# Optimization experiments

Hardware: AMD Instinct MI355X
Metric: run time of the kernel (lower is better)

The kernel has to match this reference:

```python
import jax, jax.numpy as jnp
import numpy as np

B, DIM, MID, H, W = 4, 256, 128, 128, 128
EPS = 1e-5


def _conv(x, w, pad):
    # x: [B,C,H,W], w: [O,I,k,k]
    return jax.lax.conv_general_dilated(
        x, w, window_strides=(1, 1), padding=[(pad, pad), (pad, pad)],
        dimension_numbers=('NCHW', 'OIHW', 'NCHW'))


def _bn(x, g, b, m, v):
    inv = jax.lax.rsqrt(v + EPS)
    scale = (g * inv)[None, :, None, None]
    shift = (b - m * g * inv)[None, :, None, None]
    return x * scale + shift


def _convbnrelu(x, w, g, b, m, v):
    return jax.nn.relu(_bn(_conv(x, w, 1), g, b, m, v))


# CornerNet directional pools: sequential max-accumulation scans.
def top_pool(x):     # max over y' >= y  -> reversed cummax along H
    return jax.lax.cummax(x, axis=2, reverse=True)

def bottom_pool(x):  # max over y' <= y
    return jax.lax.cummax(x, axis=2)

def left_pool(x):    # max over x' >= x
    return jax.lax.cummax(x, axis=3, reverse=True)

def right_pool(x):   # max over x' <= x
    return jax.lax.cummax(x, axis=3)


def setup_inputs() -> dict:
    key = jax.random.key(0)
    ks = jax.random.split(key, 32)
    it = iter(ks)

    def w(shape, scale=0.05):
        return jax.random.normal(next(it), shape, jnp.float32) * scale

    def bn_params(c):
        return (jnp.ones((c,), jnp.float32) + 0.1 * jax.random.normal(next(it), (c,), jnp.float32),
                0.1 * jax.random.normal(next(it), (c,), jnp.float32),
                0.1 * jax.random.normal(next(it), (c,), jnp.float32),
                jax.random.uniform(next(it), (c,), jnp.float32) + 0.5)

    inp = {'x': jax.random.normal(next(it), (B, DIM, H, W), jnp.float32)}

    inp['p1_w'] = w((MID, DIM, 3, 3))
    inp['p1_g'], inp['p1_b'], inp['p1_m'], inp['p1_v'] = bn_params(MID)
    inp['p2_w'] = w((MID, DIM, 3, 3))
    inp['p2_g'], inp['p2_b'], inp['p2_m'], inp['p2_v'] = bn_params(MID)
    inp['p_w'] = w((DIM, MID, 3, 3))
    inp['p_g'], inp['p_b'], inp['p_m'], inp['p_v'] = bn_params(DIM)
    inp['c1_w'] = w((DIM, DIM, 1, 1))
    inp['c1_g'], inp['c1_b'], inp['c1_m'], inp['c1_v'] = bn_params(DIM)
    inp['c2_w'] = w((DIM, DIM, 3, 3))
    inp['c2_g'], inp['c2_b'], inp['c2_m'], inp['c2_v'] = bn_params(DIM)
    return inp


def reference(x,
              p1_w, p1_g, p1_b, p1_m, p1_v,
              p2_w, p2_g, p2_b, p2_m, p2_v,
              p_w, p_g, p_b, p_m, p_v,
              c1_w, c1_g, c1_b, c1_m, c1_v,
              c2_w, c2_g, c2_b, c2_m, c2_v):
    # branch 1: conv-bn-relu -> top pool -> bottom pool
    pool1 = bottom_pool(top_pool(_convbnrelu(x, p1_w, p1_g, p1_b, p1_m, p1_v)))
    # branch 2: conv-bn-relu -> left pool -> right pool
    pool2 = right_pool(left_pool(_convbnrelu(x, p2_w, p2_g, p2_b, p2_m, p2_v)))
    # merge branch
    p_bn1 = _bn(_conv(pool1 + pool2, p_w, 1), p_g, p_b, p_m, p_v)
    # skip branch: 1x1 conv + bn
    bn1 = _bn(_conv(x, c1_w, 0), c1_g, c1_b, c1_m, c1_v)
    # residual add + relu, then final conv-bn-relu
    return _convbnrelu(jax.nn.relu(p_bn1 + bn1), c2_w, c2_g, c2_b, c2_m, c2_v)
```

## Files before the change

kernel.cpp:

```cpp
#include <hip/hip_runtime.h>
#include <hip/hip_bf16.h>
#include <math.h>


constexpr int NB   = 4;
constexpr int CDIM = 256;
constexpr int CMID = 128;
constexpr int HS   = 128;
constexpr int WS   = 128;
constexpr float EPS = 1e-5f;

typedef __bf16 bf16x8 __attribute__((ext_vector_type(8)));
typedef float  f32x4  __attribute__((ext_vector_type(4)));

#define AS1 __attribute__((address_space(1)))
#define AS3 __attribute__((address_space(3)))

__device__ __forceinline__ void load16_lds(const void* gsrc, void* ldst) {
    __builtin_amdgcn_global_load_lds((const AS1 unsigned int*)gsrc,
                                     (AS3 unsigned int*)ldst, 16, 0, 0);
}

__global__ __launch_bounds__(512) void k_xprep(const float* __restrict__ xin,
                                               __hip_bfloat16* __restrict__ Xc)
{
    const int y = blockIdx.x;
    const int b = blockIdx.y;
    const int t = threadIdx.x;
    __shared__ __hip_bfloat16 lds[128 * 264];
#pragma unroll
    for (int k = 0; k < 16; ++k) {
        int idx = t + k * 512;
        int ci = idx >> 5, x4 = idx & 31;
        f32x4 v = *(const f32x4*)(xin + (((size_t)b * CDIM + ci) * HS + y) * WS + x4 * 4);
#pragma unroll
        for (int j = 0; j < 4; ++j)
            lds[(x4 * 4 + j) * 264 + ci] = __float2bfloat16(v[j]);
    }
    __syncthreads();
#pragma unroll
    for (int k = 0; k < 8; ++k) {
        int i = t + k * 512;
        int x = i >> 5, c8 = i & 31;
        bf16x8 vv = *(const bf16x8*)(lds + x * 264 + c8 * 8);
        *(bf16x8*)(Xc + ((size_t)(b * 128 + y) * 128 + x) * 256 + c8 * 8) = vv;
    }
}

__global__ __launch_bounds__(256) void k_wprep_all(
    const float* __restrict__ p1w, const float* __restrict__ p2w,
    const float* __restrict__ c2w, const float* __restrict__ c1w,
    __hip_bfloat16* __restrict__ Aw1, __hip_bfloat16* __restrict__ Aw2,
    __hip_bfloat16* __restrict__ Aw5, __hip_bfloat16* __restrict__ Aw4)
{
    const int bid = blockIdx.x;
    const int t   = threadIdx.x;
    if (bid < 512) {
        const float* W; __hip_bfloat16* A; int co;
        if (bid < 128)      { W = p1w; A = Aw1; co = bid; }
        else if (bid < 256) { W = p2w; A = Aw2; co = bid - 128; }
        else                { W = c2w; A = Aw5; co = bid - 256; }
#pragma unroll
        for (int tap = 0; tap < 9; ++tap)
            A[(size_t)co * 2304 + tap * 256 + t] =
                __float2bfloat16(W[((size_t)co * CDIM + t) * 9 + tap]);
    } else {
        int base = (bid - 512) * 512 + t;
        Aw4[base]       = __float2bfloat16(c1w[base]);
        Aw4[base + 256] = __float2bfloat16(c1w[base + 256]);
    }
}

template<int MODE>
__global__ __launch_bounds__(256, 2) void k_conv3(
    const __hip_bfloat16* __restrict__ Xc,
    const __hip_bfloat16* __restrict__ Aw,
    const float* __restrict__ zbuf,
    const float* __restrict__ gg, const float* __restrict__ bbp,
    const float* __restrict__ mmp, const float* __restrict__ vvp,
    void* __restrict__ outp, int CO)
{
    const int y   = blockIdx.x;
    const int co0 = blockIdx.y * 128;
    const int b   = blockIdx.z;

    __shared__ __hip_bfloat16 smem[514 * 64];
    __shared__ float s_sc[128], s_sh[128];
    __shared__ unsigned s_red[128];
    char* smb = (char*)smem;

    const int t    = threadIdx.x;
    const int lane = t & 63;
    const int w    = t >> 6;
    const int ml   = lane & 15;
    const int q    = lane >> 4;
    const int mbase = (w >> 1) * 64;
    const int nbase = (w & 1) * 64;

    if (t < 128) {
        int co = co0 + t;
        float iv = rsqrtf(vvp[co] + EPS);
        float sc = gg[co] * iv;
        s_sc[t] = sc;
        s_sh[t] = bbp[co] - mmp[co] * sc;
        if (MODE == 2) s_red[t] = 0u;
    }

    f32x4 acc[4][4];
#pragma unroll
    for (int mt = 0; mt < 4; ++mt)
#pragma unroll
        for (int nt = 0; nt < 4; ++nt)
            acc[mt][nt] = (f32x4){0.f, 0.f, 0.f, 0.f};

#pragma unroll 1
    for (int ky = 0; ky < 3; ++ky) {
        const int ydata = y + ky - 1;
        if ((unsigned)ydata >= 128u) continue;
        const __hip_bfloat16* arow = Aw + (size_t)co0 * 2304 + (3 * ky) * 256;
        const __hip_bfloat16* brow = Xc + (size_t)(b * 128 + ydata) * 128 * 256;
#pragma unroll 1
        for (int cih = 0; cih < 4; ++cih) {
#pragma unroll
            for (int p = 0; p < 17; ++p) {
                int i = t + p * 256;
                if (i < 4112) {
                    int row = i >> 3;
                    int cl  = (i & 7) ^ (row & 7);
                    const __hip_bfloat16* src;
                    if (row < 384) {
                        int j    = row >> 7;
                        int co_l = row & 127;
                        src = arow + (size_t)co_l * 2304 + j * 256 + cih * 64 + cl * 8;
                    } else {
                        int gx = (row - 384) - 1;
                        src = ((unsigned)gx < 128u)
                            ? brow + (size_t)gx * 256 + cih * 64 + cl * 8
                            : (const __hip_bfloat16*)((const char*)zbuf + cl * 16);
                    }
                    load16_lds(src, smb + (size_t)i * 16);
                }
            }
            __syncthreads();
#pragma unroll
            for (int j = 0; j < 3; ++j) {
#pragma unroll
                for (int s = 0; s < 2; ++s) {
                    bf16x8 af[4], bfv[4];
#pragma unroll
                    for (int mt = 0; mt < 4; ++mt) {
                        const int ra = j * 128 + mbase + mt * 16 + ml;
                        const int coff = ((s * 4 + q) ^ (ra & 7)) * 16;
                        af[mt] = *(const bf16x8*)(smb + (size_t)ra * 128 + coff);
                    }
#pragma unroll
                    for (int nt = 0; nt < 4; ++nt) {
                        const int rb = 384 + nbase + nt * 16 + ml + j;
                        const int coff = ((s * 4 + q) ^ (rb & 7)) * 16;
                        bfv[nt] = *(const bf16x8*)(smb + (size_t)rb * 128 + coff);
                    }
#pragma unroll
                    for (int mt = 0; mt < 4; ++mt)
#pragma unroll
                        for (int nt = 0; nt < 4; ++nt)
                            acc[mt][nt] = __builtin_amdgcn_mfma_f32_16x16x32_bf16(
                                af[mt], bfv[nt], acc[mt][nt], 0, 0, 0);
                }
            }
            __syncthreads();
        }
    }

#pragma unroll
    for (int mt = 0; mt < 4; ++mt) {
#pragma unroll
        for (int r = 0; r < 4; ++r) {
            const int col = mbase + mt * 16 + q * 4 + r;
            const float sc = s_sc[col], sh = s_sh[col];
            const int co = co0 + col;
            unsigned rmx = 0u;
#pragma unroll
            for (int nt = 0; nt < 4; ++nt) {
                float v = fmaxf(acc[mt][nt][r] * sc + sh, 0.f);
                const int x = nbase + nt * 16 + ml;
                if (MODE == 0) {
                    ((float*)outp)[(((size_t)b * CO + co) * HS + y) * WS + x] = v;
                } else if (MODE == 1) {
                    atomicMax((unsigned*)outp + ((size_t)(b * 128 + co)) * 128 + x,
                              __float_as_uint(v));
                } else {
                    rmx = max(rmx, __float_as_uint(v));
                }
            }
            if (MODE == 2) atomicMax(&s_red[col], rmx);
        }
    }
    if (MODE == 2) {
        __syncthreads();
        if (t < 128)
            atomicMax((unsigned*)outp + ((size_t)(b * 128 + t)) * 128 + y, s_red[t]);
    }
}

__global__ __launch_bounds__(128) void k_uv(
    const float* __restrict__ pw, const float* __restrict__ cm,
    const float* __restrict__ rm,
    __hip_bfloat16* __restrict__ U, __hip_bfloat16* __restrict__ V)
{
    const int co   = blockIdx.x;
    const int b    = blockIdx.y;
    const int mode = blockIdx.z;
    const int p    = threadIdx.x;
    float acc0 = 0.f, acc1 = 0.f, acc2 = 0.f;
    const float* base = (mode == 0) ? cm : rm;
    for (int ci = 0; ci < CMID; ++ci) {
        const float* w9 = pw + (co * CMID + ci) * 9;
        float s0[3], s1[3], s2[3];
        if (mode == 0) {
#pragma unroll
            for (int k = 0; k < 3; ++k) {
                float a = w9[k], qq = w9[3 + k], r = w9[6 + k];
                s0[k] = qq + r; s1[k] = a + qq + r; s2[k] = a + qq;
            }
        } else {
#pragma unroll
            for (int k = 0; k < 3; ++k) {
                float a = w9[k*3 + 0], qq = w9[k*3 + 1], r = w9[k*3 + 2];
                s0[k] = qq + r; s1[k] = a + qq + r; s2[k] = a + qq;
            }
        }
        const float* v = base + (b * CMID + ci) * 128;
#pragma unroll
        for (int k = 0; k < 3; ++k) {
            int pos = p + k - 1;
            if ((unsigned)pos < 128u) {
                float vv = v[pos];
                acc0 += s0[k] * vv; acc1 += s1[k] * vv; acc2 += s2[k] * vv;
            }
        }
    }
    __hip_bfloat16* dst = (mode == 0) ? U : V;
    dst[((0 * NB + b) * CDIM + co) * 128 + p] = __float2bfloat16(acc0);
    dst[((1 * NB + b) * CDIM + co) * 128 + p] = __float2bfloat16(acc1);
    dst[((2 * NB + b) * CDIM + co) * 128 + p] = __float2bfloat16(acc2);
}

__global__ __launch_bounds__(256, 3) void k_merge_mfma(
    const __hip_bfloat16* __restrict__ Xc, const __hip_bfloat16* __restrict__ Aw4,
    const __hip_bfloat16* __restrict__ U, const __hip_bfloat16* __restrict__ V,
    const float* __restrict__ pg, const float* __restrict__ pb,
    const float* __restrict__ pm, const float* __restrict__ pv,
    const float* __restrict__ cg, const float* __restrict__ cb,
    const float* __restrict__ cmn, const float* __restrict__ cv,
    __hip_bfloat16* __restrict__ Rc)
{
    const int y   = blockIdx.x;
    const int cot = blockIdx.y;
    const int b   = blockIdx.z;
    const int co0 = cot * 128;
    __shared__ __hip_bfloat16 smem[256 * 64];
    __shared__ float s_psc[128], s_psh[128], s_csc[128], s_csh[128];
    __shared__ float s_v0[128], s_vm[128], s_v1[128];
    char* smb = (char*)smem;
    const int t = threadIdx.x, lane = t & 63, w = t >> 6;
    const int ml = lane & 15, q = lane >> 4;
    const int mbase = (w >> 1) * 64, nbase = (w & 1) * 64;
    const int yc = (y == 0) ? 0 : ((y == HS - 1) ? 2 : 1);

    if (t < 128) {
        int co = co0 + t;
        float iv = rsqrtf(pv[co] + EPS);
        float psc = pg[co] * iv;
        s_psc[t] = psc;
        s_psh[t] = pb[co] - pm[co] * psc;
        float iv2 = rsqrtf(cv[co] + EPS);
        float csc = cg[co] * iv2;
        s_csc[t] = csc;
        s_csh[t] = cb[co] - cmn[co] * csc;
        const size_t vb = ((size_t)b * CDIM + co) * 128 + y;
        const size_t cstr = (size_t)NB * CDIM * 128;
        s_v0[t] = __bfloat162float(V[vb]);
        s_vm[t] = __bfloat162float(V[cstr + vb]);
        s_v1[t] = __bfloat162float(V[2 * cstr + vb]);
    }

    f32x4 acc[4][4];
#pragma unroll
    for (int mt = 0; mt < 4; ++mt)
#pragma unroll
        for (int nt = 0; nt < 4; ++nt)
            acc[mt][nt] = (f32x4){0.f, 0.f, 0.f, 0.f};

    const __hip_bfloat16* brow = Xc + (size_t)(b * 128 + y) * 128 * 256;
#pragma unroll 1
    for (int ks = 0; ks < 4; ++ks) {
        const __hip_bfloat16* ab = Aw4 + (size_t)co0 * 256 + ks * 64;
        const __hip_bfloat16* bb = brow + ks * 64;
#pragma unroll
        for (int p = 0; p < 8; ++p) {
            int i   = t + p * 256;
            int row = i >> 3;
            int c   = (i & 7) ^ (row & 7);
            const __hip_bfloat16* src = (row < 128)
                ? ab + (size_t)row * 256 + c * 8
                : bb + (size_t)(row - 128) * 256 + c * 8;
            load16_lds(src, smb + (size_t)i * 16);
        }
        __syncthreads();
#pragma unroll
        for (int s = 0; s < 2; ++s) {
            const int coff = ((s * 4 + q) ^ (ml & 7)) * 16;
            bf16x8 af[4], bfv[4];
#pragma unroll
            for (int mt = 0; mt < 4; ++mt)
                af[mt] = *(const bf16x8*)(smb + (size_t)(mbase + mt * 16 + ml) * 128 + coff);
#pragma unroll
            for (int nt = 0; nt < 4; ++nt)
                bfv[nt] = *(const bf16x8*)(smb + (size_t)(128 + nbase + nt * 16 + ml) * 128 + coff);
#pragma unroll
            for (int mt = 0; mt < 4; ++mt)
#pragma unroll
                for (int nt = 0; nt < 4; ++nt)
                    acc[mt][nt] = __builtin_amdgcn_mfma_f32_16x16x32_bf16(
                        af[mt], bfv[nt], acc[mt][nt], 0, 0, 0);
        }
        __syncthreads();
    }

    const __hip_bfloat16* Ub = U + ((size_t)(yc * NB + b) * CDIM + co0) * 128;
#pragma unroll
    for (int p = 0; p < 8; ++p) {
        int i = t + p * 256;
        load16_lds(Ub + (size_t)i * 8, smb + (size_t)i * 16);
    }
    __syncthreads();

#pragma unroll
    for (int mt = 0; mt < 4; ++mt) {
#pragma unroll
        for (int nt = 0; nt < 4; ++nt) {
            const int x = nbase + nt * 16 + ml;
            unsigned long long pk = 0;
#pragma unroll
            for (int r = 0; r < 4; ++r) {
                const int col = mbase + mt * 16 + q * 4 + r;
                float u  = __bfloat162float(smem[col * 128 + x]);
                float vt = (x == 0) ? s_v0[col] : ((x == WS - 1) ? s_v1[col] : s_vm[col]);
                float val = fmaxf((u + vt) * s_psc[col] + s_psh[col]
                                  + acc[mt][nt][r] * s_csc[col] + s_csh[col], 0.f);
                __hip_bfloat16 hb = __float2bfloat16(val);
                unsigned short bits;
                __builtin_memcpy(&bits, &hb, 2);
                pk |= (unsigned long long)bits << (16 * r);
            }
            *(unsigned long long*)((char*)Rc +
                ((size_t)((b * 128 + y) * 128 + x) * 256 + co0 + mbase + mt * 16 + q * 4) * 2) = pk;
        }
    }
}

extern "C" void kernel_launch(void* const* d_in, const int* in_sizes, int n_in,
                              void* d_out, int out_size, void* d_ws, size_t ws_size,
                              hipStream_t stream)
{
    (void)in_sizes; (void)n_in; (void)out_size; (void)ws_size;
    const float* x    = (const float*)d_in[0];
    const float* p1_w = (const float*)d_in[1];
    const float* p1_g = (const float*)d_in[2];
    const float* p1_b = (const float*)d_in[3];
    const float* p1_m = (const float*)d_in[4];
    const float* p1_v = (const float*)d_in[5];
    const float* p2_w = (const float*)d_in[6];
    const float* p2_g = (const float*)d_in[7];
    const float* p2_b = (const float*)d_in[8];
    const float* p2_m = (const float*)d_in[9];
    const float* p2_v = (const float*)d_in[10];
    const float* p_w  = (const float*)d_in[11];
    const float* p_g  = (const float*)d_in[12];
    const float* p_b  = (const float*)d_in[13];
    const float* p_m  = (const float*)d_in[14];
    const float* p_v  = (const float*)d_in[15];
    const float* c1_w = (const float*)d_in[16];
    const float* c1_g = (const float*)d_in[17];
    const float* c1_b = (const float*)d_in[18];
    const float* c1_m = (const float*)d_in[19];
    const float* c1_v = (const float*)d_in[20];
    const float* c2_w = (const float*)d_in[21];
    const float* c2_g = (const float*)d_in[22];
    const float* c2_b = (const float*)d_in[23];
    const float* c2_m = (const float*)d_in[24];
    const float* c2_v = (const float*)d_in[25];
    float* out = (float*)d_out;
    char* ws = (char*)d_ws;

    __hip_bfloat16* Xc   = (__hip_bfloat16*)ws;
    __hip_bfloat16* Rc   = (__hip_bfloat16*)(ws + 33554432);
    __hip_bfloat16* Ubuf = (__hip_bfloat16*)(ws + 67108864);
    __hip_bfloat16* Vbuf = (__hip_bfloat16*)(ws + 67895296);
    __hip_bfloat16* Aw1  = (__hip_bfloat16*)(ws + 67108864);
    __hip_bfloat16* Aw2  = (__hip_bfloat16*)(ws + 67698688);
    __hip_bfloat16* Aw5  = (__hip_bfloat16*)(ws + 68681728);
    __hip_bfloat16* Aw4  = (__hip_bfloat16*)(ws + 69861376);
    unsigned*       cmaxU = (unsigned*)(ws + 69992448);
    unsigned*       rmaxU = (unsigned*)(ws + 70254592);
    float*          zbuf  = (float*)(ws + 70516736);

    hipMemsetAsync(ws + 69992448, 0, 524544, stream);
    k_xprep<<<dim3(128, 4), 512, 0, stream>>>(x, Xc);
    k_wprep_all<<<dim3(640), 256, 0, stream>>>(
        p1_w, p2_w, c2_w, c1_w, Aw1, Aw2, Aw5, Aw4);

    k_conv3<1><<<dim3(128, 1, 4), 256, 0, stream>>>(
        Xc, Aw1, zbuf, p1_g, p1_b, p1_m, p1_v, cmaxU, CMID);
    k_conv3<2><<<dim3(128, 1, 4), 256, 0, stream>>>(
        Xc, Aw2, zbuf, p2_g, p2_b, p2_m, p2_v, rmaxU, CMID);

    k_uv<<<dim3(256, 4, 2), 128, 0, stream>>>(
        p_w, (const float*)cmaxU, (const float*)rmaxU, Ubuf, Vbuf);

    k_merge_mfma<<<dim3(128, 2, 4), 256, 0, stream>>>(
        Xc, Aw4, Ubuf, Vbuf, p_g, p_b, p_m, p_v,
        c1_g, c1_b, c1_m, c1_v, Rc);

    k_conv3<0><<<dim3(128, 2, 4), 256, 0, stream>>>(
        Rc, Aw5, zbuf, c2_g, c2_b, c2_m, c2_v, out, CDIM);
}
```

Measured before the change: 425.3 us.

## Compute two output rows per conv block and merge both pool-branch convs into one launch

```diff
diff --git a/kernel.cpp b/kernel.cpp
--- a/kernel.cpp
+++ b/kernel.cpp
@@ -74,19 +74,29 @@
 template<int MODE>
 __global__ __launch_bounds__(256, 2) void k_conv3(
     const __hip_bfloat16* __restrict__ Xc,
-    const __hip_bfloat16* __restrict__ Aw,
+    const __hip_bfloat16* __restrict__ AwA, const __hip_bfloat16* __restrict__ AwB,
     const float* __restrict__ zbuf,
-    const float* __restrict__ gg, const float* __restrict__ bbp,
-    const float* __restrict__ mmp, const float* __restrict__ vvp,
-    void* __restrict__ outp, int CO)
-{
-    const int y   = blockIdx.x;
-    const int co0 = blockIdx.y * 128;
-    const int b   = blockIdx.z;
-
-    __shared__ __hip_bfloat16 smem[514 * 64];
+    const float* __restrict__ g1, const float* __restrict__ b1,
+    const float* __restrict__ m1, const float* __restrict__ v1,
+    const float* __restrict__ g2, const float* __restrict__ b2,
+    const float* __restrict__ m2, const float* __restrict__ v2,
+    float* __restrict__ out0, unsigned* __restrict__ cmax,
+    unsigned* __restrict__ rmax, int CO)
+{
+    const int y0     = blockIdx.x * 2;
+    const int branch = blockIdx.y;
+    const int b      = blockIdx.z;
+    const int co0    = (MODE == 0) ? branch * 128 : 0;
+
+    const __hip_bfloat16* Aw = (MODE == 1 && branch) ? AwB : AwA;
+    const float* gg  = (MODE == 1 && branch) ? g2 : g1;
+    const float* bbp = (MODE == 1 && branch) ? b2 : b1;
+    const float* mmp = (MODE == 1 && branch) ? m2 : m1;
+    const float* vvp = (MODE == 1 && branch) ? v2 : v1;
+
+    __shared__ __hip_bfloat16 smem[644 * 32];
     __shared__ float s_sc[128], s_sh[128];
-    __shared__ unsigned s_red[128];
+    __shared__ unsigned s_red[2][128];
     char* smb = (char*)smem;
 
     const int t    = threadIdx.x;
@@ -103,40 +113,44 @@
         float sc = gg[co] * iv;
         s_sc[t] = sc;
         s_sh[t] = bbp[co] - mmp[co] * sc;
-        if (MODE == 2) s_red[t] = 0u;
-    }
-
-    f32x4 acc[4][4];
-#pragma unroll
-    for (int mt = 0; mt < 4; ++mt)
-#pragma unroll
-        for (int nt = 0; nt < 4; ++nt)
-            acc[mt][nt] = (f32x4){0.f, 0.f, 0.f, 0.f};
+        if (MODE == 1) { s_red[0][t] = 0u; s_red[1][t] = 0u; }
+    }
+
+    f32x4 acc[2][4][4];
+#pragma unroll
+    for (int yy = 0; yy < 2; ++yy)
+#pragma unroll
+        for (int mt = 0; mt < 4; ++mt)
+#pragma unroll
+            for (int nt = 0; nt < 4; ++nt)
+                acc[yy][mt][nt] = (f32x4){0.f, 0.f, 0.f, 0.f};
+
+    const __hip_bfloat16* bbase = Xc + (size_t)(b * 128) * 128 * 256;
 
 #pragma unroll 1
     for (int ky = 0; ky < 3; ++ky) {
-        const int ydata = y + ky - 1;
-        if ((unsigned)ydata >= 128u) continue;
+        const int yd0 = y0 + ky - 1;
         const __hip_bfloat16* arow = Aw + (size_t)co0 * 2304 + (3 * ky) * 256;
-        const __hip_bfloat16* brow = Xc + (size_t)(b * 128 + ydata) * 128 * 256;
 #pragma unroll 1
-        for (int cih = 0; cih < 4; ++cih) {
-#pragma unroll
-            for (int p = 0; p < 17; ++p) {
+        for (int cih = 0; cih < 8; ++cih) {
+            const int cb = cih * 32;
+#pragma unroll
+            for (int p = 0; p < 11; ++p) {
                 int i = t + p * 256;
-                if (i < 4112) {
-                    int row = i >> 3;
-                    int cl  = (i & 7) ^ (row & 7);
+                if (i < 2576) {
+                    int row = i >> 2, c = i & 3;
                     const __hip_bfloat16* src;
                     if (row < 384) {
-                        int j    = row >> 7;
-                        int co_l = row & 127;
-                        src = arow + (size_t)co_l * 2304 + j * 256 + cih * 64 + cl * 8;
+                        int j = row >> 7, col = row & 127;
+                        src = arow + (size_t)col * 2304 + j * 256 + cb + c * 8;
                     } else {
-                        int gx = (row - 384) - 1;
-                        src = ((unsigned)gx < 128u)
-                            ? brow + (size_t)gx * 256 + cih * 64 + cl * 8
-                            : (const __hip_bfloat16*)((const char*)zbuf + cl * 16);
+                        int rbi = row - 384;
+                        int yy  = rbi >= 130;
+                        int xi  = rbi - 130 * yy;
+                        int gy  = yd0 + yy, gx = xi - 1;
+                        src = ((unsigned)gy < 128u && (unsigned)gx < 128u)
+                            ? bbase + ((size_t)(gy * 128 + gx)) * 256 + cb + c * 8
+                            : (const __hip_bfloat16*)((const char*)zbuf + c * 16);
                     }
                     load16_lds(src, smb + (size_t)i * 16);
                 }
@@ -144,27 +158,24 @@
             __syncthreads();
 #pragma unroll
             for (int j = 0; j < 3; ++j) {
-#pragma unroll
-                for (int s = 0; s < 2; ++s) {
-                    bf16x8 af[4], bfv[4];
-#pragma unroll
-                    for (int mt = 0; mt < 4; ++mt) {
-                        const int ra = j * 128 + mbase + mt * 16 + ml;
-                        const int coff = ((s * 4 + q) ^ (ra & 7)) * 16;
-                        af[mt] = *(const bf16x8*)(smb + (size_t)ra * 128 + coff);
-                    }
-#pragma unroll
-                    for (int nt = 0; nt < 4; ++nt) {
-                        const int rb = 384 + nbase + nt * 16 + ml + j;
-                        const int coff = ((s * 4 + q) ^ (rb & 7)) * 16;
-                        bfv[nt] = *(const bf16x8*)(smb + (size_t)rb * 128 + coff);
-                    }
+                bf16x8 af[4];
+#pragma unroll
+                for (int mt = 0; mt < 4; ++mt)
+                    af[mt] = *(const bf16x8*)(smb +
+                        (size_t)(j * 128 + mbase + mt * 16 + ml) * 64 + q * 16);
+#pragma unroll
+                for (int yy = 0; yy < 2; ++yy) {
+                    bf16x8 bfv[4];
+#pragma unroll
+                    for (int nt = 0; nt < 4; ++nt)
+                        bfv[nt] = *(const bf16x8*)(smb +
+                            (size_t)(384 + yy * 130 + nbase + nt * 16 + ml + j) * 64 + q * 16);
 #pragma unroll
                     for (int mt = 0; mt < 4; ++mt)
 #pragma unroll
                         for (int nt = 0; nt < 4; ++nt)
-                            acc[mt][nt] = __builtin_amdgcn_mfma_f32_16x16x32_bf16(
-                                af[mt], bfv[nt], acc[mt][nt], 0, 0, 0);
+                            acc[yy][mt][nt] = __builtin_amdgcn_mfma_f32_16x16x32_bf16(
+                                af[mt], bfv[nt], acc[yy][mt][nt], 0, 0, 0);
                 }
             }
             __syncthreads();
@@ -178,27 +189,35 @@
             const int col = mbase + mt * 16 + q * 4 + r;
             const float sc = s_sc[col], sh = s_sh[col];
             const int co = co0 + col;
-            unsigned rmx = 0u;
+            unsigned rmx0 = 0u, rmx1 = 0u;
 #pragma unroll
             for (int nt = 0; nt < 4; ++nt) {
-                float v = fmaxf(acc[mt][nt][r] * sc + sh, 0.f);
+                float va = fmaxf(acc[0][mt][nt][r] * sc + sh, 0.f);
+                float vb = fmaxf(acc[1][mt][nt][r] * sc + sh, 0.f);
                 const int x = nbase + nt * 16 + ml;
                 if (MODE == 0) {
-                    ((float*)outp)[(((size_t)b * CO + co) * HS + y) * WS + x] = v;
-                } else if (MODE == 1) {
-                    atomicMax((unsigned*)outp + ((size_t)(b * 128 + co)) * 128 + x,
-                              __float_as_uint(v));
+                    out0[(((size_t)b * CO + co) * HS + y0)     * WS + x] = va;
+                    out0[(((size_t)b * CO + co) * HS + y0 + 1) * WS + x] = vb;
+                } else if (branch == 0) {
+                    atomicMax(cmax + ((size_t)(b * 128 + co)) * 128 + x,
+                              __float_as_uint(fmaxf(va, vb)));
                 } else {
-                    rmx = max(rmx, __float_as_uint(v));
+                    rmx0 = max(rmx0, __float_as_uint(va));
+                    rmx1 = max(rmx1, __float_as_uint(vb));
                 }
             }
-            if (MODE == 2) atomicMax(&s_red[col], rmx);
-        }
-    }
-    if (MODE == 2) {
+            if (MODE == 1 && branch == 1) {
+                atomicMax(&s_red[0][col], rmx0);
+                atomicMax(&s_red[1][col], rmx1);
+            }
+        }
+    }
+    if (MODE == 1 && branch == 1) {
         __syncthreads();
-        if (t < 128)
-            atomicMax((unsigned*)outp + ((size_t)(b * 128 + t)) * 128 + y, s_red[t]);
+        if (t < 128) {
+            atomicMax(rmax + ((size_t)(b * 128 + t)) * 128 + y0,     s_red[0][t]);
+            atomicMax(rmax + ((size_t)(b * 128 + t)) * 128 + y0 + 1, s_red[1][t]);
+        }
     }
 }
 
@@ -410,10 +429,10 @@
     k_wprep_all<<<dim3(640), 256, 0, stream>>>(
         p1_w, p2_w, c2_w, c1_w, Aw1, Aw2, Aw5, Aw4);
 
-    k_conv3<1><<<dim3(128, 1, 4), 256, 0, stream>>>(
-        Xc, Aw1, zbuf, p1_g, p1_b, p1_m, p1_v, cmaxU, CMID);
-    k_conv3<2><<<dim3(128, 1, 4), 256, 0, stream>>>(
-        Xc, Aw2, zbuf, p2_g, p2_b, p2_m, p2_v, rmaxU, CMID);
+    k_conv3<1><<<dim3(64, 2, 4), 256, 0, stream>>>(
+        Xc, Aw1, Aw2, zbuf,
+        p1_g, p1_b, p1_m, p1_v, p2_g, p2_b, p2_m, p2_v,
+        nullptr, cmaxU, rmaxU, CMID);
 
     k_uv<<<dim3(256, 4, 2), 128, 0, stream>>>(
         p_w, (const float*)cmaxU, (const float*)rmaxU, Ubuf, Vbuf);
@@ -422,6 +441,8 @@
         Xc, Aw4, Ubuf, Vbuf, p_g, p_b, p_m, p_v,
         c1_g, c1_b, c1_m, c1_v, Rc);
 
-    k_conv3<0><<<dim3(128, 2, 4), 256, 0, stream>>>(
-        Rc, Aw5, zbuf, c2_g, c2_b, c2_m, c2_v, out, CDIM);
-}
+    k_conv3<0><<<dim3(64, 2, 4), 256, 0, stream>>>(
+        Rc, Aw5, nullptr, zbuf,
+        c2_g, c2_b, c2_m, c2_v, nullptr, nullptr, nullptr, nullptr,
+        out, nullptr, nullptr, CDIM);
+}
```

After: 392.7 us. 7.7% less time.
